# Kernel optimization log

Hardware: AMD Instinct MI355X
Metric: run time of the kernel (lower is better)

The kernel has to match this reference:

```python
import jax, jax.numpy as jnp
import numpy as np

EMBED = 1024
HEADS = 16
HEAD_DIM = EMBED // HEADS


def setup_inputs() -> dict:
    key = jax.random.key(0)
    ks = jax.random.split(key, 9)
    s = 1.0 / np.sqrt(EMBED)
    x = jax.random.normal(ks[0], (2, 2048, EMBED), dtype=jnp.float32)
    Wq = jax.random.uniform(ks[1], (EMBED, EMBED), jnp.float32, -s, s)
    bq = jax.random.uniform(ks[2], (EMBED,), jnp.float32, -s, s)
    Wk = jax.random.uniform(ks[3], (EMBED, EMBED), jnp.float32, -s, s)
    bk = jax.random.uniform(ks[4], (EMBED,), jnp.float32, -s, s)
    Wv = jax.random.uniform(ks[5], (EMBED, EMBED), jnp.float32, -s, s)
    bv = jax.random.uniform(ks[6], (EMBED,), jnp.float32, -s, s)
    Wo = jax.random.uniform(ks[7], (EMBED, EMBED), jnp.float32, -s, s)
    bo = jax.random.uniform(ks[8], (EMBED,), jnp.float32, -s, s)
    return {"x": x, "Wq": Wq, "bq": bq, "Wk": Wk, "bk": bk,
            "Wv": Wv, "bv": bv, "Wo": Wo, "bo": bo}


def reference(x, Wq, bq, Wk, bk, Wv, bv, Wo, bo):
    B, S, E = x.shape
    H, D = HEADS, HEAD_DIM
    # QKV projections, split heads: [B,S,E] -> [B,H,S,D]
    def proj(W, b):
        return (x @ W + b).reshape(B, S, H, D).transpose(0, 2, 1, 3)
    q, k, v = proj(Wq, bq), proj(Wk, bk), proj(Wv, bv)
    scores = jnp.einsum('bhsd,bhtd->bhst', q, k) / jnp.sqrt(jnp.float32(D))
    attn = jax.nn.softmax(scores, axis=-1)
    out = jnp.einsum('bhst,bhtd->bhsd', attn, v)  # [B,H,S,D]
    out = out.transpose(0, 2, 1, 3).reshape(B, S, E)
    return out @ Wo + bo
```

## Files before the change

kernel.cpp:

```cpp
#include <hip/hip_runtime.h>
#include <cstddef>
#include <cstdint>

#define EMB 1024
#define NH 16
#define HD 64
#define SEQ 2048
#define BATCH 2
#define MROWS 4096

typedef unsigned short u16;
typedef __attribute__((ext_vector_type(8))) short short8;
typedef __attribute__((ext_vector_type(4))) short short4v;
typedef __attribute__((ext_vector_type(4))) float floatx4;

#define MFMA32(a,b,c) __builtin_amdgcn_mfma_f32_16x16x32_bf16((a),(b),(c),0,0,0)

#if __has_builtin(__builtin_amdgcn_mfma_f32_16x16x16bf16_1k)
#define PVMFMA(a,b,c) __builtin_amdgcn_mfma_f32_16x16x16bf16_1k((a),(b),(c),0,0,0)
#elif __has_builtin(__builtin_amdgcn_mfma_f32_16x16x16_bf16)
#define PVMFMA(a,b,c) __builtin_amdgcn_mfma_f32_16x16x16_bf16((a),(b),(c),0,0,0)
#else
__device__ __forceinline__ floatx4 pv_mfma_fb(short4v a, short4v b, floatx4 c) {
    short8 a8 = {a.x, a.y, a.z, a.w, 0, 0, 0, 0};
    short8 b8 = {b.x, b.y, b.z, b.w, 0, 0, 0, 0};
    return MFMA32(a8, b8, c);
}
#define PVMFMA(a,b,c) pv_mfma_fb((a),(b),(c))
#endif

__device__ __forceinline__ u16 f2bf(float f) {
    union { float f; uint32_t u; } v; v.f = f;
    return (u16)((v.u + 0x7fffu + ((v.u >> 16) & 1u)) >> 16);
}
__device__ __forceinline__ uint32_t pk_trunc(float a, float b) {
    union { float f; uint32_t u; } va, vb; va.f = a; vb.f = b;
    return __builtin_amdgcn_perm(vb.u, va.u, 0x07060302u);
}
typedef const __attribute__((address_space(1))) void* gptr_t;
typedef __attribute__((address_space(3))) void* lptr_t;
__device__ __forceinline__ void gl2lds16(const void* g, void* l) {
    __builtin_amdgcn_global_load_lds((gptr_t)g, (lptr_t)l, 16, 0, 0);
}

__global__ __launch_bounds__(256) void cvt_x_k(const float* __restrict__ x,
                                               u16* __restrict__ xh) {
    const int stride = gridDim.x * 256 * 8;
    for (int i = (blockIdx.x * 256 + threadIdx.x) * 8; i < MROWS * EMB; i += stride) {
        float4 a = *(const float4*)(x + i);
        float4 b = *(const float4*)(x + i + 4);
        alignas(16) u16 o[8] = {f2bf(a.x), f2bf(a.y), f2bf(a.z), f2bf(a.w),
                                f2bf(b.x), f2bf(b.y), f2bf(b.z), f2bf(b.w)};
        *(uint4*)(xh + i) = *(const uint4*)o;
    }
}

__global__ __launch_bounds__(256) void cvt_wt_k(
    const float* __restrict__ W0, const float* __restrict__ W1,
    const float* __restrict__ W2, const float* __restrict__ W3,
    u16* __restrict__ Wt4) {
    const int z = blockIdx.z;
    const float* W = (z == 0) ? W0 : (z == 1) ? W1 : (z == 2) ? W2 : W3;
    const float scale = (z == 0) ? 0.125f : 1.0f;
    u16* dst = Wt4 + (size_t)z * 1048576;
    __shared__ float Lf[64][65];
    const int kt = blockIdx.y * 64, nt = blockIdx.x * 64;
    const int tid = threadIdx.x;
    {
        const int r = tid >> 2, c4 = (tid & 3) * 16;
        const float* src = W + (size_t)(kt + r) * EMB + nt + c4;
        #pragma unroll
        for (int i = 0; i < 16; i += 4) {
            float4 v = *(const float4*)(src + i);
            Lf[r][c4 + i + 0] = v.x; Lf[r][c4 + i + 1] = v.y;
            Lf[r][c4 + i + 2] = v.z; Lf[r][c4 + i + 3] = v.w;
        }
    }
    __syncthreads();
    const int n = tid >> 2, k4 = (tid & 3) * 16;
    alignas(16) u16 hb[16];
    #pragma unroll
    for (int i = 0; i < 16; ++i) hb[i] = f2bf(Lf[k4 + i][n] * scale);
    const size_t o = (size_t)(nt + n) * EMB + kt + k4;
    *(uint4*)(dst + o) = *(const uint4*)hb;
    *(uint4*)(dst + o + 8) = *(const uint4*)(hb + 8);
}

__global__ __launch_bounds__(256) void gemm_qkv_k(
    const u16* __restrict__ xh, const u16* __restrict__ Wt4,
    const float* __restrict__ b0, const float* __restrict__ b1,
    const float* __restrict__ b2,
    u16* __restrict__ Q, u16* __restrict__ K, u16* __restrict__ V) {
    const int z = blockIdx.z;
    const u16* Wt = Wt4 + (size_t)z * 1048576;
    const float* bias = (z == 0) ? b0 : (z == 1) ? b1 : b2;
    u16* out = (z == 0) ? Q : (z == 1) ? K : V;
    const float bscale = (z == 0) ? 0.125f : 1.0f;
    const int bm = blockIdx.y * 128, bn = blockIdx.x * 128;
    __shared__ alignas(16) u16 As[4096];
    __shared__ alignas(16) u16 Bs[4096];
    const int tid = threadIdx.x;
    const int lane = tid & 63, w = tid >> 6;
    const int l15 = lane & 15, quad = lane >> 4;
    const int wm = (w & 1) * 64, wn = (w >> 1) * 64;

    floatx4 acc[4][4];
    const floatx4 zf = {0.f, 0.f, 0.f, 0.f};
    #pragma unroll
    for (int mt = 0; mt < 4; ++mt)
        #pragma unroll
        for (int nt = 0; nt < 4; ++nt) acc[mt][nt] = zf;

    const int c0 = tid, c1 = tid + 256;
    const int r0 = c0 >> 2, p0 = c0 & 3, cc0 = (p0 - r0 - (r0 >> 2)) & 3;
    const int r1 = c1 >> 2, p1 = c1 & 3, cc1 = (p1 - r1 - (r1 >> 2)) & 3;
    const u16* ag0 = xh + (size_t)(bm + r0) * EMB + cc0 * 8;
    const u16* ag1 = xh + (size_t)(bm + r1) * EMB + cc1 * 8;
    const u16* bg0 = Wt + (size_t)(bn + r0) * EMB + cc0 * 8;
    const u16* bg1 = Wt + (size_t)(bn + r1) * EMB + cc1 * 8;

    for (int kt = 0; kt < EMB; kt += 32) {
        __syncthreads();
        gl2lds16(ag0 + kt, &As[c0 * 8]); gl2lds16(ag1 + kt, &As[c1 * 8]);
        gl2lds16(bg0 + kt, &Bs[c0 * 8]); gl2lds16(bg1 + kt, &Bs[c1 * 8]);
        __syncthreads();
        short8 af[4], bf[4];
        #pragma unroll
        for (int t = 0; t < 4; ++t) {
            const int ra = wm + t * 16 + l15;
            const int rb = wn + t * 16 + l15;
            af[t] = *(const short8*)&As[ra * 32 + ((quad + ra + (ra >> 2)) & 3) * 8];
            bf[t] = *(const short8*)&Bs[rb * 32 + ((quad + rb + (rb >> 2)) & 3) * 8];
        }
        #pragma unroll
        for (int mt = 0; mt < 4; ++mt)
            #pragma unroll
            for (int nt = 0; nt < 4; ++nt)
                acc[mt][nt] = MFMA32(af[mt], bf[nt], acc[mt][nt]);
    }

    #pragma unroll
    for (int nt = 0; nt < 4; ++nt) {
        const int col = bn + wn + nt * 16 + l15;
        const float bv = bias[col] * bscale;
        #pragma unroll
        for (int mt = 0; mt < 4; ++mt) {
            const int row = bm + wm + mt * 16 + quad * 4;
            #pragma unroll
            for (int r = 0; r < 4; ++r)
                out[(size_t)(row + r) * EMB + col] = f2bf(acc[mt][nt][r] + bv);
        }
    }
}

__global__ __launch_bounds__(256) void gemm_o_k(
    const u16* __restrict__ Ag, const u16* __restrict__ Wt,
    const float* __restrict__ bias, float* __restrict__ out) {
    const int bm = blockIdx.y * 128, bn = blockIdx.x * 128;
    __shared__ alignas(16) u16 As[4096];
    __shared__ alignas(16) u16 Bs[4096];
    const int tid = threadIdx.x;
    const int lane = tid & 63, w = tid >> 6;
    const int l15 = lane & 15, quad = lane >> 4;
    const int wm = (w & 1) * 64, wn = (w >> 1) * 64;

    floatx4 acc[4][4];
    const floatx4 zf = {0.f, 0.f, 0.f, 0.f};
    #pragma unroll
    for (int mt = 0; mt < 4; ++mt)
        #pragma unroll
        for (int nt = 0; nt < 4; ++nt) acc[mt][nt] = zf;

    const int c0 = tid, c1 = tid + 256;
    const int r0 = c0 >> 2, p0 = c0 & 3, cc0 = (p0 - r0 - (r0 >> 2)) & 3;
    const int r1 = c1 >> 2, p1 = c1 & 3, cc1 = (p1 - r1 - (r1 >> 2)) & 3;
    const u16* ag0 = Ag + (size_t)(bm + r0) * EMB + cc0 * 8;
    const u16* ag1 = Ag + (size_t)(bm + r1) * EMB + cc1 * 8;
    const u16* bg0 = Wt + (size_t)(bn + r0) * EMB + cc0 * 8;
    const u16* bg1 = Wt + (size_t)(bn + r1) * EMB + cc1 * 8;

    for (int kt = 0; kt < EMB; kt += 32) {
        __syncthreads();
        gl2lds16(ag0 + kt, &As[c0 * 8]); gl2lds16(ag1 + kt, &As[c1 * 8]);
        gl2lds16(bg0 + kt, &Bs[c0 * 8]); gl2lds16(bg1 + kt, &Bs[c1 * 8]);
        __syncthreads();
        short8 af[4], bf[4];
        #pragma unroll
        for (int t = 0; t < 4; ++t) {
            const int ra = wm + t * 16 + l15;
            const int rb = wn + t * 16 + l15;
            af[t] = *(const short8*)&As[ra * 32 + ((quad + ra + (ra >> 2)) & 3) * 8];
            bf[t] = *(const short8*)&Bs[rb * 32 + ((quad + rb + (rb >> 2)) & 3) * 8];
        }
        #pragma unroll
        for (int mt = 0; mt < 4; ++mt)
            #pragma unroll
            for (int nt = 0; nt < 4; ++nt)
                acc[mt][nt] = MFMA32(af[mt], bf[nt], acc[mt][nt]);
    }

    #pragma unroll
    for (int nt = 0; nt < 4; ++nt) {
        const int col = bn + wn + nt * 16 + l15;
        const float bv = bias[col];
        #pragma unroll
        for (int mt = 0; mt < 4; ++mt) {
            const int row = bm + wm + mt * 16 + quad * 4;
            #pragma unroll
            for (int r = 0; r < 4; ++r)
                out[(size_t)(row + r) * EMB + col] = acc[mt][nt][r] + bv;
        }
    }
}

__global__ __launch_bounds__(256) void vtrans_k(const u16* __restrict__ V,
                                                u16* __restrict__ Vt) {
    const int tt = blockIdx.x, h = blockIdx.y, b = blockIdx.z;
    __shared__ u16 Lt[64][72];
    const int tid = threadIdx.x;
    {
        const int r = tid >> 2, c4 = (tid & 3) * 16;
        const u16* src = V + (size_t)(b * SEQ + tt * 64 + r) * EMB + h * HD + c4;
        alignas(16) u16 buf[16];
        *(uint4*)buf = *(const uint4*)src;
        *(uint4*)(buf + 8) = *(const uint4*)(src + 8);
        #pragma unroll
        for (int i = 0; i < 16; ++i) Lt[c4 + i][r] = buf[i];
    }
    __syncthreads();
    const int d = tid >> 2, t4 = (tid & 3) * 16;
    u16* dst = Vt + ((size_t)((b * NH + h) * HD + d)) * SEQ + tt * 64 + t4;
    *(uint4*)dst = *(const uint4*)&Lt[d][t4];
    *(uint4*)(dst + 8) = *(const uint4*)&Lt[d][t4 + 8];
}

__global__ __launch_bounds__(256) void flash_k(
    const u16* __restrict__ Q, const u16* __restrict__ K,
    const u16* __restrict__ Vt, u16* __restrict__ AO) {
    const int qt = blockIdx.x, h = blockIdx.y, b = blockIdx.z;
    __shared__ alignas(16) u16 Ks[4096];
    __shared__ alignas(16) u16 Vs[4096];
    const int tid = threadIdx.x;
    const int lane = tid & 63, w = tid >> 6;
    const int l15 = lane & 15, quad = lane >> 4;

    const u16* qp = Q + (size_t)(b * SEQ + qt * 64 + w * 16 + l15) * EMB + h * HD + quad * 8;
    const short8 qb0 = *(const short8*)qp;
    const short8 qb1 = *(const short8*)(qp + 32);

    const floatx4 zf = {0.f, 0.f, 0.f, 0.f};
    floatx4 oacc[4];
    #pragma unroll
    for (int nt = 0; nt < 4; ++nt) oacc[nt] = zf;
    float l_part = 0.f;

    const int s0 = tid, s1 = tid + 256;
    const int kr0 = s0 >> 3, kc0 = ((s0 & 7) - kr0) & 7;
    const int kr1 = s1 >> 3, kc1 = ((s1 & 7) - kr1) & 7;
    const u16* kg0 = K + (size_t)(b * SEQ + kr0) * EMB + h * HD + kc0 * 8;
    const u16* kg1 = K + (size_t)(b * SEQ + kr1) * EMB + h * HD + kc1 * 8;
    const u16* vg0 = Vt + ((size_t)((b * NH + h) * HD + kr0)) * SEQ + kc0 * 8;
    const u16* vg1 = Vt + ((size_t)((b * NH + h) * HD + kr1)) * SEQ + kc1 * 8;

    for (int kt = 0; kt < SEQ / 64; ++kt) {
        __syncthreads();
        gl2lds16(kg0 + (size_t)kt * 64 * EMB, &Ks[s0 * 8]);
        gl2lds16(kg1 + (size_t)kt * 64 * EMB, &Ks[s1 * 8]);
        gl2lds16(vg0 + kt * 64, &Vs[s0 * 8]);
        gl2lds16(vg1 + kt * 64, &Vs[s1 * 8]);
        __syncthreads();

        floatx4 sa[4];
        #pragma unroll
        for (int mt = 0; mt < 4; ++mt) {
            const int r = mt * 16 + l15;
            const short8 ka0 = *(const short8*)&Ks[r * 64 + ((quad + r) & 7) * 8];
            const short8 ka1 = *(const short8*)&Ks[r * 64 + ((quad + 4 + r) & 7) * 8];
            sa[mt] = MFMA32(ka1, qb1, MFMA32(ka0, qb0, zf));
        }

        short4v pfr[4];
        #pragma unroll
        for (int mt = 0; mt < 4; ++mt) {
            const float e0 = __expf(sa[mt][0]);
            const float e1 = __expf(sa[mt][1]);
            const float e2 = __expf(sa[mt][2]);
            const float e3 = __expf(sa[mt][3]);
            const uint32_t u01 = pk_trunc(e0, e1);
            const uint32_t u23 = pk_trunc(e2, e3);
            union { float f; uint32_t u; } a, bb, c, d;
            a.u = u01 << 16; bb.u = u01 & 0xffff0000u;
            c.u = u23 << 16; d.u = u23 & 0xffff0000u;
            l_part += (a.f + bb.f) + (c.f + d.f);
            union { uint32_t u[2]; short4v s; } pk;
            pk.u[0] = u01; pk.u[1] = u23;
            pfr[mt] = pk.s;
        }

        #pragma unroll
        for (int mt = 0; mt < 4; ++mt) {
            const int c16 = mt * 2 + (quad >> 1);
            const int hof = (quad & 1) * 4;
            #pragma unroll
            for (int nt = 0; nt < 4; ++nt) {
                const int vr = nt * 16 + l15;
                const short4v vb =
                    *(const short4v*)&Vs[vr * 64 + ((c16 + vr) & 7) * 8 + hof];
                oacc[nt] = PVMFMA(pfr[mt], vb, oacc[nt]);
            }
        }
    }

    l_part += __shfl_xor(l_part, 16, 64);
    l_part += __shfl_xor(l_part, 32, 64);

    #pragma unroll
    for (int r = 0; r < 4; ++r) {
        const float lq = __shfl(l_part, quad * 4 + r, 16);
        const float inv = 1.f / lq;
        const size_t o =
            (size_t)(b * SEQ + qt * 64 + w * 16 + quad * 4 + r) * EMB + h * HD + l15;
        #pragma unroll
        for (int nt = 0; nt < 4; ++nt)
            AO[o + nt * 16] = f2bf(oacc[nt][r] * inv);
    }
}

extern "C" void kernel_launch(void* const* d_in, const int* in_sizes, int n_in,
                              void* d_out, int out_size, void* d_ws, size_t ws_size,
                              hipStream_t stream) {
    const float* x  = (const float*)d_in[0];
    const float* Wq = (const float*)d_in[1];
    const float* bq = (const float*)d_in[2];
    const float* Wk = (const float*)d_in[3];
    const float* bk = (const float*)d_in[4];
    const float* Wv = (const float*)d_in[5];
    const float* bv = (const float*)d_in[6];
    const float* Wo = (const float*)d_in[7];
    const float* bo = (const float*)d_in[8];

    u16* ws16 = (u16*)d_ws;
    const size_t P4 = (size_t)MROWS * EMB;
    u16* xh  = ws16;
    u16* Qb  = ws16 + P4;
    u16* Kb  = ws16 + 2 * P4;
    u16* Vb  = ws16 + 3 * P4;
    u16* Vtb = ws16 + 4 * P4;
    u16* Wt4 = ws16 + 5 * P4;

    cvt_x_k<<<1024, 256, 0, stream>>>(x, xh);
    cvt_wt_k<<<dim3(16, 16, 4), 256, 0, stream>>>(Wq, Wk, Wv, Wo, Wt4);
    gemm_qkv_k<<<dim3(8, 32, 3), 256, 0, stream>>>(xh, Wt4, bq, bk, bv, Qb, Kb, Vb);
    vtrans_k<<<dim3(32, 16, 2), 256, 0, stream>>>(Vb, Vtb);
    flash_k<<<dim3(32, 16, 2), 256, 0, stream>>>(Qb, Kb, Vtb, xh);
    gemm_o_k<<<dim3(8, 32, 1), 256, 0, stream>>>(xh, Wt4 + 3 * 1048576, bo, (float*)d_out);
}
```

Baseline: 214.1 us.

## Split attention KV range across blocks, add reduce pass, exp2 softmax, narrower O-proj tiles

```diff
diff --git a/kernel.cpp b/kernel.cpp
--- a/kernel.cpp
+++ b/kernel.cpp
@@ -8,6 +8,7 @@
 #define SEQ 2048
 #define BATCH 2
 #define MROWS 4096
+#define LOG2E 1.4426950408889634f
 
 typedef unsigned short u16;
 typedef __attribute__((ext_vector_type(8))) short short8;
@@ -37,6 +38,12 @@
     union { float f; uint32_t u; } va, vb; va.f = a; vb.f = b;
     return __builtin_amdgcn_perm(vb.u, va.u, 0x07060302u);
 }
+__device__ __forceinline__ float lo_f(uint32_t u) {
+    union { uint32_t u; float f; } v; v.u = u << 16; return v.f;
+}
+__device__ __forceinline__ float hi_f(uint32_t u) {
+    union { uint32_t u; float f; } v; v.u = u & 0xffff0000u; return v.f;
+}
 typedef const __attribute__((address_space(1))) void* gptr_t;
 typedef __attribute__((address_space(3))) void* lptr_t;
 __device__ __forceinline__ void gl2lds16(const void* g, void* l) {
@@ -61,7 +68,7 @@
     u16* __restrict__ Wt4) {
     const int z = blockIdx.z;
     const float* W = (z == 0) ? W0 : (z == 1) ? W1 : (z == 2) ? W2 : W3;
-    const float scale = (z == 0) ? 0.125f : 1.0f;
+    const float scale = (z == 0) ? 0.125f * LOG2E : 1.0f;
     u16* dst = Wt4 + (size_t)z * 1048576;
     __shared__ float Lf[64][65];
     const int kt = blockIdx.y * 64, nt = blockIdx.x * 64;
@@ -95,7 +102,7 @@
     const u16* Wt = Wt4 + (size_t)z * 1048576;
     const float* bias = (z == 0) ? b0 : (z == 1) ? b1 : b2;
     u16* out = (z == 0) ? Q : (z == 1) ? K : V;
-    const float bscale = (z == 0) ? 0.125f : 1.0f;
+    const float bscale = (z == 0) ? 0.125f * LOG2E : 1.0f;
     const int bm = blockIdx.y * 128, bn = blockIdx.x * 128;
     __shared__ alignas(16) u16 As[4096];
     __shared__ alignas(16) u16 Bs[4096];
@@ -156,18 +163,18 @@
 __global__ __launch_bounds__(256) void gemm_o_k(
     const u16* __restrict__ Ag, const u16* __restrict__ Wt,
     const float* __restrict__ bias, float* __restrict__ out) {
-    const int bm = blockIdx.y * 128, bn = blockIdx.x * 128;
+    const int bm = blockIdx.y * 128, bn = blockIdx.x * 64;
     __shared__ alignas(16) u16 As[4096];
-    __shared__ alignas(16) u16 Bs[4096];
+    __shared__ alignas(16) u16 Bs[2048];
     const int tid = threadIdx.x;
     const int lane = tid & 63, w = tid >> 6;
     const int l15 = lane & 15, quad = lane >> 4;
-    const int wm = (w & 1) * 64, wn = (w >> 1) * 64;
-
-    floatx4 acc[4][4];
+    const int wm = w * 32;
+
+    floatx4 acc[2][4];
     const floatx4 zf = {0.f, 0.f, 0.f, 0.f};
     #pragma unroll
-    for (int mt = 0; mt < 4; ++mt)
+    for (int mt = 0; mt < 2; ++mt)
         #pragma unroll
         for (int nt = 0; nt < 4; ++nt) acc[mt][nt] = zf;
 
@@ -177,23 +184,26 @@
     const u16* ag0 = Ag + (size_t)(bm + r0) * EMB + cc0 * 8;
     const u16* ag1 = Ag + (size_t)(bm + r1) * EMB + cc1 * 8;
     const u16* bg0 = Wt + (size_t)(bn + r0) * EMB + cc0 * 8;
-    const u16* bg1 = Wt + (size_t)(bn + r1) * EMB + cc1 * 8;
 
     for (int kt = 0; kt < EMB; kt += 32) {
         __syncthreads();
-        gl2lds16(ag0 + kt, &As[c0 * 8]); gl2lds16(ag1 + kt, &As[c1 * 8]);
-        gl2lds16(bg0 + kt, &Bs[c0 * 8]); gl2lds16(bg1 + kt, &Bs[c1 * 8]);
-        __syncthreads();
-        short8 af[4], bf[4];
+        gl2lds16(ag0 + kt, &As[c0 * 8]);
+        gl2lds16(ag1 + kt, &As[c1 * 8]);
+        if (c0 < 256) gl2lds16(bg0 + kt, &Bs[c0 * 8]);
+        __syncthreads();
+        short8 af[2], bf[4];
+        #pragma unroll
+        for (int t = 0; t < 2; ++t) {
+            const int ra = wm + t * 16 + l15;
+            af[t] = *(const short8*)&As[ra * 32 + ((quad + ra + (ra >> 2)) & 3) * 8];
+        }
         #pragma unroll
         for (int t = 0; t < 4; ++t) {
-            const int ra = wm + t * 16 + l15;
-            const int rb = wn + t * 16 + l15;
-            af[t] = *(const short8*)&As[ra * 32 + ((quad + ra + (ra >> 2)) & 3) * 8];
+            const int rb = t * 16 + l15;
             bf[t] = *(const short8*)&Bs[rb * 32 + ((quad + rb + (rb >> 2)) & 3) * 8];
         }
         #pragma unroll
-        for (int mt = 0; mt < 4; ++mt)
+        for (int mt = 0; mt < 2; ++mt)
             #pragma unroll
             for (int nt = 0; nt < 4; ++nt)
                 acc[mt][nt] = MFMA32(af[mt], bf[nt], acc[mt][nt]);
@@ -201,10 +211,10 @@
 
     #pragma unroll
     for (int nt = 0; nt < 4; ++nt) {
-        const int col = bn + wn + nt * 16 + l15;
+        const int col = bn + nt * 16 + l15;
         const float bv = bias[col];
         #pragma unroll
-        for (int mt = 0; mt < 4; ++mt) {
+        for (int mt = 0; mt < 2; ++mt) {
             const int row = bm + wm + mt * 16 + quad * 4;
             #pragma unroll
             for (int r = 0; r < 4; ++r)
@@ -236,33 +246,41 @@
 
 __global__ __launch_bounds__(256) void flash_k(
     const u16* __restrict__ Q, const u16* __restrict__ K,
-    const u16* __restrict__ Vt, u16* __restrict__ AO) {
-    const int qt = blockIdx.x, h = blockIdx.y, b = blockIdx.z;
+    const u16* __restrict__ Vt, u16* __restrict__ Np0, u16* __restrict__ Np1,
+    float* __restrict__ Lp) {
+    const int qt = blockIdx.x, h = blockIdx.y;
+    const int b = blockIdx.z >> 1, half = blockIdx.z & 1;
+    const int t0 = half * (SEQ / 2);
     __shared__ alignas(16) u16 Ks[4096];
     __shared__ alignas(16) u16 Vs[4096];
     const int tid = threadIdx.x;
     const int lane = tid & 63, w = tid >> 6;
     const int l15 = lane & 15, quad = lane >> 4;
 
-    const u16* qp = Q + (size_t)(b * SEQ + qt * 64 + w * 16 + l15) * EMB + h * HD + quad * 8;
-    const short8 qb0 = *(const short8*)qp;
-    const short8 qb1 = *(const short8*)(qp + 32);
+    const u16* qp = Q + (size_t)(b * SEQ + qt * 128 + w * 32 + l15) * EMB + h * HD + quad * 8;
+    short8 qb[2][2];
+    qb[0][0] = *(const short8*)qp;
+    qb[0][1] = *(const short8*)(qp + 32);
+    qb[1][0] = *(const short8*)(qp + 16 * EMB);
+    qb[1][1] = *(const short8*)(qp + 16 * EMB + 32);
 
     const floatx4 zf = {0.f, 0.f, 0.f, 0.f};
-    floatx4 oacc[4];
-    #pragma unroll
-    for (int nt = 0; nt < 4; ++nt) oacc[nt] = zf;
-    float l_part = 0.f;
+    floatx4 oacc[2][4];
+    float l_part[2] = {0.f, 0.f};
+    #pragma unroll
+    for (int u = 0; u < 2; ++u)
+        #pragma unroll
+        for (int nt = 0; nt < 4; ++nt) oacc[u][nt] = zf;
 
     const int s0 = tid, s1 = tid + 256;
     const int kr0 = s0 >> 3, kc0 = ((s0 & 7) - kr0) & 7;
     const int kr1 = s1 >> 3, kc1 = ((s1 & 7) - kr1) & 7;
-    const u16* kg0 = K + (size_t)(b * SEQ + kr0) * EMB + h * HD + kc0 * 8;
-    const u16* kg1 = K + (size_t)(b * SEQ + kr1) * EMB + h * HD + kc1 * 8;
-    const u16* vg0 = Vt + ((size_t)((b * NH + h) * HD + kr0)) * SEQ + kc0 * 8;
-    const u16* vg1 = Vt + ((size_t)((b * NH + h) * HD + kr1)) * SEQ + kc1 * 8;
-
-    for (int kt = 0; kt < SEQ / 64; ++kt) {
+    const u16* kg0 = K + (size_t)(b * SEQ + t0 + kr0) * EMB + h * HD + kc0 * 8;
+    const u16* kg1 = K + (size_t)(b * SEQ + t0 + kr1) * EMB + h * HD + kc1 * 8;
+    const u16* vg0 = Vt + ((size_t)((b * NH + h) * HD + kr0)) * SEQ + t0 + kc0 * 8;
+    const u16* vg1 = Vt + ((size_t)((b * NH + h) * HD + kr1)) * SEQ + t0 + kc1 * 8;
+
+    for (int kt = 0; kt < SEQ / 2 / 64; ++kt) {
         __syncthreads();
         gl2lds16(kg0 + (size_t)kt * 64 * EMB, &Ks[s0 * 8]);
         gl2lds16(kg1 + (size_t)kt * 64 * EMB, &Ks[s1 * 8]);
@@ -270,32 +288,33 @@
         gl2lds16(vg1 + kt * 64, &Vs[s1 * 8]);
         __syncthreads();
 
-        floatx4 sa[4];
+        floatx4 sa[2][4];
         #pragma unroll
         for (int mt = 0; mt < 4; ++mt) {
             const int r = mt * 16 + l15;
             const short8 ka0 = *(const short8*)&Ks[r * 64 + ((quad + r) & 7) * 8];
             const short8 ka1 = *(const short8*)&Ks[r * 64 + ((quad + 4 + r) & 7) * 8];
-            sa[mt] = MFMA32(ka1, qb1, MFMA32(ka0, qb0, zf));
-        }
-
-        short4v pfr[4];
-        #pragma unroll
-        for (int mt = 0; mt < 4; ++mt) {
-            const float e0 = __expf(sa[mt][0]);
-            const float e1 = __expf(sa[mt][1]);
-            const float e2 = __expf(sa[mt][2]);
-            const float e3 = __expf(sa[mt][3]);
-            const uint32_t u01 = pk_trunc(e0, e1);
-            const uint32_t u23 = pk_trunc(e2, e3);
-            union { float f; uint32_t u; } a, bb, c, d;
-            a.u = u01 << 16; bb.u = u01 & 0xffff0000u;
-            c.u = u23 << 16; d.u = u23 & 0xffff0000u;
-            l_part += (a.f + bb.f) + (c.f + d.f);
-            union { uint32_t u[2]; short4v s; } pk;
-            pk.u[0] = u01; pk.u[1] = u23;
-            pfr[mt] = pk.s;
-        }
+            #pragma unroll
+            for (int u = 0; u < 2; ++u)
+                sa[u][mt] = MFMA32(ka1, qb[u][1], MFMA32(ka0, qb[u][0], zf));
+        }
+
+        short4v pfr[2][4];
+        #pragma unroll
+        for (int u = 0; u < 2; ++u)
+            #pragma unroll
+            for (int mt = 0; mt < 4; ++mt) {
+                const float e0 = exp2f(sa[u][mt][0]);
+                const float e1 = exp2f(sa[u][mt][1]);
+                const float e2 = exp2f(sa[u][mt][2]);
+                const float e3 = exp2f(sa[u][mt][3]);
+                const uint32_t u01 = pk_trunc(e0, e1);
+                const uint32_t u23 = pk_trunc(e2, e3);
+                l_part[u] += (lo_f(u01) + hi_f(u01)) + (lo_f(u23) + hi_f(u23));
+                union { uint32_t uu[2]; short4v s; } pk;
+                pk.uu[0] = u01; pk.uu[1] = u23;
+                pfr[u][mt] = pk.s;
+            }
 
         #pragma unroll
         for (int mt = 0; mt < 4; ++mt) {
@@ -306,24 +325,58 @@
                 const int vr = nt * 16 + l15;
                 const short4v vb =
                     *(const short4v*)&Vs[vr * 64 + ((c16 + vr) & 7) * 8 + hof];
-                oacc[nt] = PVMFMA(pfr[mt], vb, oacc[nt]);
+                #pragma unroll
+                for (int u = 0; u < 2; ++u)
+                    oacc[u][nt] = PVMFMA(pfr[u][mt], vb, oacc[u][nt]);
             }
         }
     }
 
-    l_part += __shfl_xor(l_part, 16, 64);
-    l_part += __shfl_xor(l_part, 32, 64);
-
-    #pragma unroll
-    for (int r = 0; r < 4; ++r) {
-        const float lq = __shfl(l_part, quad * 4 + r, 16);
-        const float inv = 1.f / lq;
-        const size_t o =
-            (size_t)(b * SEQ + qt * 64 + w * 16 + quad * 4 + r) * EMB + h * HD + l15;
-        #pragma unroll
-        for (int nt = 0; nt < 4; ++nt)
-            AO[o + nt * 16] = f2bf(oacc[nt][r] * inv);
-    }
+    u16* np = half ? Np1 : Np0;
+    float* lp = Lp + (size_t)half * (MROWS * NH);
+
+    #pragma unroll
+    for (int u = 0; u < 2; ++u) {
+        l_part[u] += __shfl_xor(l_part[u], 16, 64);
+        l_part[u] += __shfl_xor(l_part[u], 32, 64);
+        if (quad == 0) {
+            const int qrow = qt * 128 + w * 32 + u * 16 + l15;
+            lp[(size_t)(b * SEQ + qrow) * NH + h] = l_part[u];
+        }
+    }
+
+    #pragma unroll
+    for (int u = 0; u < 2; ++u)
+        #pragma unroll
+        for (int r = 0; r < 4; ++r) {
+            const size_t o =
+                (size_t)(b * SEQ + qt * 128 + w * 32 + u * 16 + quad * 4 + r) * EMB
+                + h * HD + l15;
+            #pragma unroll
+            for (int nt = 0; nt < 4; ++nt)
+                np[o + nt * 16] = f2bf(oacc[u][nt][r]);
+        }
+}
+
+__global__ __launch_bounds__(256) void reduce_k(
+    const u16* __restrict__ Np0, const u16* __restrict__ Np1,
+    const float* __restrict__ Lp, u16* __restrict__ AO) {
+    const int i = blockIdx.x * 256 + threadIdx.x;
+    const int e = i * 4;
+    const int row = e >> 10;
+    const int hh = (e & 1023) >> 6;
+    const float inv =
+        1.f / (Lp[(size_t)row * NH + hh] + Lp[(size_t)MROWS * NH + (size_t)row * NH + hh]);
+    const uint2 n0 = *(const uint2*)(Np0 + e);
+    const uint2 n1 = *(const uint2*)(Np1 + e);
+    const float x0 = (lo_f(n0.x) + lo_f(n1.x)) * inv;
+    const float x1 = (hi_f(n0.x) + hi_f(n1.x)) * inv;
+    const float x2 = (lo_f(n0.y) + lo_f(n1.y)) * inv;
+    const float x3 = (hi_f(n0.y) + hi_f(n1.y)) * inv;
+    uint2 o;
+    o.x = (uint32_t)f2bf(x0) | ((uint32_t)f2bf(x1) << 16);
+    o.y = (uint32_t)f2bf(x2) | ((uint32_t)f2bf(x3) << 16);
+    *(uint2*)(AO + e) = o;
 }
 
 extern "C" void kernel_launch(void* const* d_in, const int* in_sizes, int n_in,
@@ -347,11 +400,13 @@
     u16* Vb  = ws16 + 3 * P4;
     u16* Vtb = ws16 + 4 * P4;
     u16* Wt4 = ws16 + 5 * P4;
+    float* Lp = (float*)(ws16 + 6 * P4);
 
     cvt_x_k<<<1024, 256, 0, stream>>>(x, xh);
     cvt_wt_k<<<dim3(16, 16, 4), 256, 0, stream>>>(Wq, Wk, Wv, Wo, Wt4);
     gemm_qkv_k<<<dim3(8, 32, 3), 256, 0, stream>>>(xh, Wt4, bq, bk, bv, Qb, Kb, Vb);
     vtrans_k<<<dim3(32, 16, 2), 256, 0, stream>>>(Vb, Vtb);
-    flash_k<<<dim3(32, 16, 2), 256, 0, stream>>>(Qb, Kb, Vtb, xh);
-    gemm_o_k<<<dim3(8, 32, 1), 256, 0, stream>>>(xh, Wt4 + 3 * 1048576, bo, (float*)d_out);
-}
+    flash_k<<<dim3(16, 16, 4), 256, 0, stream>>>(Qb, Kb, Vtb, xh, Vb, Lp);
+    reduce_k<<<4096, 256, 0, stream>>>(xh, Vb, Lp, Qb);
+    gemm_o_k<<<dim3(16, 32, 1), 256, 0, stream>>>(Qb, Wt4 + 3 * 1048576, bo, (float*)d_out);
+}
```

New measurement: 222.8 us. +4.1%, slower.
